# Performance work log

Hardware: AMD Instinct MI355X
Metric: run time of the kernel (lower is better)

The kernel has to match this reference:

```python
import jax, jax.numpy as jnp
import numpy as np

N_NODES = 50000
N_EDGES = 800000
N_GRAPHS = 64
IN_C, HID, OUT_C = 128, 96, 96
EPS = 1e-5


def gcn_conv(x, W, b, src, dst, n_nodes):
    # PyG GCNConv: linear -> symmetric-normalized aggregation with self-loops
    h = x @ W  # [N, C]
    deg = jax.ops.segment_sum(jnp.ones(src.shape[0], h.dtype), dst, num_segments=n_nodes) + 1.0  # +1 self-loop
    dinv = jax.lax.rsqrt(deg)  # deg >= 1, no inf
    norm = dinv[src] * dinv[dst]  # [E]
    agg = jax.ops.segment_sum(h[src] * norm[:, None], dst, num_segments=n_nodes)
    agg = agg + h * (dinv * dinv)[:, None]  # self-loop contribution
    return agg + b


def graph_norm(x, w, b, alpha, batch, n_graphs):
    # PyG GraphNorm: per-graph mean (scaled by learnable alpha) and variance
    cnt = jax.ops.segment_sum(jnp.ones(x.shape[0], x.dtype), batch, num_segments=n_graphs)[:, None]
    mean = jax.ops.segment_sum(x, batch, num_segments=n_graphs) / cnt
    xc = x - alpha * mean[batch]
    var = jax.ops.segment_sum(xc * xc, batch, num_segments=n_graphs) / cnt
    return w * xc * jax.lax.rsqrt(var[batch] + EPS) + b


def setup_inputs() -> dict:
    key = jax.random.key(0)
    ks = jax.random.split(key, 8)
    x = jax.random.normal(ks[0], (N_NODES, IN_C), jnp.float32)
    edge_index = jax.random.randint(ks[1], (2, N_EDGES), 0, N_NODES, jnp.int64)
    batch = jnp.sort(jax.random.randint(ks[2], (N_NODES,), 0, N_GRAPHS, jnp.int64))
    s1 = 1.0 / np.sqrt(IN_C)
    s2 = 1.0 / np.sqrt(HID)
    return {
        "x": x,
        "edge_index": edge_index,
        "batch": batch,
        "W1": jax.random.uniform(ks[3], (IN_C, HID), jnp.float32, -s1, s1),
        "b1": jnp.zeros((HID,), jnp.float32),
        "gn1_w": jnp.ones((HID,), jnp.float32),
        "gn1_b": jnp.zeros((HID,), jnp.float32),
        "gn1_a": jnp.ones((HID,), jnp.float32),
        "W2": jax.random.uniform(ks[4], (HID, OUT_C), jnp.float32, -s2, s2),
        "b2": jnp.zeros((OUT_C,), jnp.float32),
        "gn2_w": jnp.ones((OUT_C,), jnp.float32),
        "gn2_b": jnp.zeros((OUT_C,), jnp.float32),
        "gn2_a": jnp.ones((OUT_C,), jnp.float32),
    }


def reference(x, edge_index, batch, W1, b1, gn1_w, gn1_b, gn1_a, W2, b2, gn2_w, gn2_b, gn2_a):
    src, dst = edge_index[0], edge_index[1]
    h = gcn_conv(x, W1, b1, src, dst, N_NODES)
    h = graph_norm(h, gn1_w, gn1_b, gn1_a, batch, N_GRAPHS)
    h = jax.nn.relu(h)  # dropout = identity in eval mode
    h = gcn_conv(h, W2, b2, src, dst, N_NODES)
    h = graph_norm(h, gn2_w, gn2_b, gn2_a, batch, N_GRAPHS)
    h = jax.nn.relu(h)
    return h
```

## Files before the change

### kernel.cpp

```cpp
#include <hip/hip_runtime.h>
#include <hip/hip_bf16.h>

#define N_NODES 50000
#define N_EDGES 800000
#define N_GRAPHS 64
#define IN_C 128
#define HID 96
#define SLICES 8
#define NBUCK 196
#define NCHK 200
#define EPC 4000

typedef short s16x8 __attribute__((ext_vector_type(8)));
typedef float f32x4 __attribute__((ext_vector_type(4)));

__device__ inline unsigned short f2bf(float f) {
    union { __hip_bfloat16 b; unsigned short u; } cv;
    cv.b = __float2bfloat16(f);
    return cv.u;
}
__device__ inline float bf2f(unsigned short u) { return __uint_as_float((unsigned int)u << 16); }
__device__ inline float bf_lo(unsigned int u) { return __uint_as_float(u << 16); }
__device__ inline float bf_hi(unsigned int u) { return __uint_as_float(u & 0xffff0000u); }


__global__ void bounds_kernel(const int* __restrict__ batch, int* __restrict__ gstart,
                              int* __restrict__ gend, int n) {
    int i = blockIdx.x * blockDim.x + threadIdx.x;
    if (i >= n) return;
    int g = batch[i];
    if (i == 0) {
        gstart[g] = 0;
    } else {
        int gp = batch[i - 1];
        if (gp != g) { gstart[g] = i; gend[gp] = i - 1; }
    }
    if (i == n - 1) gend[g] = n - 1;
}

__global__ __launch_bounds__(256)
void p1_hist(const int* __restrict__ dst, int* __restrict__ chunkHist) {
    __shared__ int h[NBUCK];
    int c = blockIdx.x, t = threadIdx.x;
    for (int i = t; i < NBUCK; i += 256) h[i] = 0;
    __syncthreads();
    int base = c * EPC;
    for (int i = t; i < EPC; i += 256)
        atomicAdd(&h[dst[base + i] >> 8], 1);
    __syncthreads();
    for (int i = t; i < NBUCK; i += 256) chunkHist[c * NBUCK + i] = h[i];
}

__global__ __launch_bounds__(256)
void p2_offsets(const int* __restrict__ chunkHist, int* __restrict__ offTab,
                int* __restrict__ bucketBase, int* __restrict__ rowstart) {
    __shared__ int sh[256];
    int t = threadIdx.x;
    int tot = 0;
    if (t < NBUCK)
        for (int c = 0; c < NCHK; ++c) tot += chunkHist[c * NBUCK + t];
    sh[t] = (t < NBUCK) ? tot : 0;
    __syncthreads();
    for (int off = 1; off < 256; off <<= 1) {
        int x = (t >= off) ? sh[t - off] : 0;
        __syncthreads();
        sh[t] += x;
        __syncthreads();
    }
    if (t < NBUCK) {
        int bb = sh[t] - tot;
        bucketBase[t] = bb;
        int run = bb;
        for (int c = 0; c < NCHK; ++c) {
            offTab[c * NBUCK + t] = run;
            run += chunkHist[c * NBUCK + t];
        }
    }
    if (t == 0) { bucketBase[NBUCK] = N_EDGES; rowstart[N_NODES] = N_EDGES; }
}

__global__ __launch_bounds__(256)
void p3_place(const int* __restrict__ src, const int* __restrict__ dst,
              const int* __restrict__ offTab, unsigned int* __restrict__ epacked) {
    __shared__ int cur[NBUCK];
    int c = blockIdx.x, t = threadIdx.x;
    for (int i = t; i < NBUCK; i += 256) cur[i] = offTab[c * NBUCK + i];
    __syncthreads();
    int base = c * EPC;
    for (int i = t; i < EPC; i += 256) {
        int d = dst[base + i];
        int s = src[base + i];
        int pos = atomicAdd(&cur[d >> 8], 1);
        epacked[pos] = ((unsigned)(d & 255) << 16) | (unsigned)s;
    }
}

__global__ __launch_bounds__(256)
void p4_fine(const unsigned int* __restrict__ epacked, const int* __restrict__ bucketBase,
             int* __restrict__ rowstart, float* __restrict__ dinv,
             unsigned short* __restrict__ e_src16) {
    __shared__ int h[256];
    __shared__ int rs[256];
    __shared__ unsigned short sorted[8192];
    int b = blockIdx.x, t = threadIdx.x;
    int s0 = bucketBase[b], len = bucketBase[b + 1] - s0;
    h[t] = 0;
    __syncthreads();
    for (int i = t; i < len; i += 256)
        atomicAdd(&h[(epacked[s0 + i] >> 16) & 255], 1);
    __syncthreads();
    int deg = h[t];
    int v = deg;
    rs[t] = v;
    __syncthreads();
    for (int off = 1; off < 256; off <<= 1) {
        int x = (t >= off) ? rs[t - off] : 0;
        __syncthreads();
        rs[t] += x;
        __syncthreads();
    }
    int myrow = rs[t] - deg;
    int node = b * 256 + t;
    if (node < N_NODES) {
        rowstart[node] = s0 + myrow;
        dinv[node] = rsqrtf((float)deg + 1.0f);
    }
    __syncthreads();
    h[t] = myrow;
    __syncthreads();
    for (int i = t; i < len; i += 256) {
        unsigned int p = epacked[s0 + i];
        int pos = atomicAdd(&h[(p >> 16) & 255], 1);
        sorted[pos] = (unsigned short)(p & 0xffffu);
    }
    __syncthreads();
    for (int i = t; i < len; i += 256) e_src16[s0 + i] = sorted[i];
}

template <int K, bool PRENORM>
__global__ __launch_bounds__(256)
void gemm_mfma(const void* __restrict__ Xv, const float* __restrict__ W,
               const float* __restrict__ dinv, const int* __restrict__ batch,
               const float* __restrict__ gA, const float* __restrict__ gB,
               unsigned short* __restrict__ Hp) {
    constexpr int KP = K + 8;
    constexpr int KS = K / 32;
    __shared__ unsigned short Wt[96 * KP];
    int tid = threadIdx.x;
    for (int idx = tid; idx < K * 96; idx += 256) {
        int k = idx / 96, c = idx - k * 96;
        Wt[c * KP + k] = f2bf(W[idx]);
    }
    __syncthreads();

    const int lane = tid & 63;
    const int quad = lane >> 4;
    const int l16 = lane & 15;

    s16x8 Bf[6][KS];
#pragma unroll
    for (int t = 0; t < 6; ++t)
#pragma unroll
        for (int s = 0; s < KS; ++s)
            Bf[t][s] = *(const s16x8*)&Wt[(t * 16 + l16) * KP + s * 32 + quad * 8];

    int gw = blockIdx.x * 4 + (tid >> 6);
    int nw = gridDim.x * 4;
    for (int tile = gw; tile < N_NODES / 16; tile += nw) {
        int n0 = tile * 16;
        int row = n0 + l16;
        s16x8 Af[KS];
        if (!PRENORM) {
            const float* Xr = (const float*)Xv + (size_t)row * K;
#pragma unroll
            for (int s = 0; s < KS; ++s) {
                int k0 = s * 32 + quad * 8;
                float4 u = *(const float4*)(Xr + k0);
                float4 v = *(const float4*)(Xr + k0 + 4);
                s16x8 a;
                a[0] = (short)f2bf(u.x); a[1] = (short)f2bf(u.y);
                a[2] = (short)f2bf(u.z); a[3] = (short)f2bf(u.w);
                a[4] = (short)f2bf(v.x); a[5] = (short)f2bf(v.y);
                a[6] = (short)f2bf(v.z); a[7] = (short)f2bf(v.w);
                Af[s] = a;
            }
        } else {
            const unsigned short* Xr = (const unsigned short*)Xv + (size_t)row * HID;
            int g = batch[row];
            const float* ga = gA + g * HID;
            const float* gb = gB + g * HID;
#pragma unroll
            for (int s = 0; s < KS; ++s) {
                int k0 = s * 32 + quad * 8;
                uint4 raw = *(const uint4*)(Xr + k0);
                float4 a0 = *(const float4*)(ga + k0);
                float4 a1 = *(const float4*)(ga + k0 + 4);
                float4 b0 = *(const float4*)(gb + k0);
                float4 b1 = *(const float4*)(gb + k0 + 4);
                s16x8 a;
                a[0] = (short)f2bf(fmaxf(fmaf(bf_lo(raw.x), a0.x, b0.x), 0.f));
                a[1] = (short)f2bf(fmaxf(fmaf(bf_hi(raw.x), a0.y, b0.y), 0.f));
                a[2] = (short)f2bf(fmaxf(fmaf(bf_lo(raw.y), a0.z, b0.z), 0.f));
                a[3] = (short)f2bf(fmaxf(fmaf(bf_hi(raw.y), a0.w, b0.w), 0.f));
                a[4] = (short)f2bf(fmaxf(fmaf(bf_lo(raw.z), a1.x, b1.x), 0.f));
                a[5] = (short)f2bf(fmaxf(fmaf(bf_hi(raw.z), a1.y, b1.y), 0.f));
                a[6] = (short)f2bf(fmaxf(fmaf(bf_lo(raw.w), a1.z, b1.z), 0.f));
                a[7] = (short)f2bf(fmaxf(fmaf(bf_hi(raw.w), a1.w, b1.w), 0.f));
                Af[s] = a;
            }
        }
        f32x4 acc[6];
#pragma unroll
        for (int t = 0; t < 6; ++t) { acc[t][0] = 0.f; acc[t][1] = 0.f; acc[t][2] = 0.f; acc[t][3] = 0.f; }
#pragma unroll
        for (int s = 0; s < KS; ++s)
#pragma unroll
            for (int t = 0; t < 6; ++t)
                acc[t] = __builtin_amdgcn_mfma_f32_16x16x32_bf16(Af[s], Bf[t][s], acc[t], 0, 0, 0);

        float4 dv = *(const float4*)(dinv + n0 + quad * 4);
#pragma unroll
        for (int t = 0; t < 6; ++t) {
            size_t base = (size_t)(n0 + quad * 4) * HID + t * 16 + l16;
            Hp[base]            = f2bf(acc[t][0] * dv.x);
            Hp[base + HID]      = f2bf(acc[t][1] * dv.y);
            Hp[base + 2 * HID]  = f2bf(acc[t][2] * dv.z);
            Hp[base + 3 * HID]  = f2bf(acc[t][3] * dv.w);
        }
    }
}

__global__ __launch_bounds__(384)
void agg_kernel(const int* __restrict__ rowstart, const unsigned short* __restrict__ e_src,
                const float* __restrict__ dinv, const unsigned short* __restrict__ H,
                const float* __restrict__ bias, unsigned short* __restrict__ OUT) {
    int node = blockIdx.x * 16 + threadIdx.y;
    int x = threadIdx.x;
    const ushort4* H4 = (const ushort4*)H;
    size_t ridx = (size_t)node * 24 + x;
    ushort4 hv = H4[ridx];
    float ax = bf2f(hv.x), ay = bf2f(hv.y), az = bf2f(hv.z), aw = bf2f(hv.w);
    int s0 = rowstart[node], s1 = rowstart[node + 1];
    int i = s0;
    for (; i + 2 <= s1; i += 2) {
        int sA = e_src[i], sB = e_src[i + 1];
        ushort4 a4 = H4[(size_t)sA * 24 + x];
        ushort4 b4 = H4[(size_t)sB * 24 + x];
        ax += bf2f(a4.x); ay += bf2f(a4.y); az += bf2f(a4.z); aw += bf2f(a4.w);
        ax += bf2f(b4.x); ay += bf2f(b4.y); az += bf2f(b4.z); aw += bf2f(b4.w);
    }
    if (i < s1) {
        int sA = e_src[i];
        ushort4 a4 = H4[(size_t)sA * 24 + x];
        ax += bf2f(a4.x); ay += bf2f(a4.y); az += bf2f(a4.z); aw += bf2f(a4.w);
    }
    float di = dinv[node];
    float4 bb = ((const float4*)bias)[x];
    ushort4 ov;
    ov.x = f2bf(fmaf(ax, di, bb.x));
    ov.y = f2bf(fmaf(ay, di, bb.y));
    ov.z = f2bf(fmaf(az, di, bb.z));
    ov.w = f2bf(fmaf(aw, di, bb.w));
    ((ushort4*)OUT)[ridx] = ov;
}


__global__ __launch_bounds__(768)
void gn_partial(const unsigned short* __restrict__ Xb, const int* __restrict__ gstart,
                const int* __restrict__ gend, float* __restrict__ gSum, float* __restrict__ gSq) {
    __shared__ float4 sSum[32][24];
    __shared__ float4 sSq[32][24];
    int g = blockIdx.x, sl = blockIdx.y;
    int x = threadIdx.x, ty = threadIdx.y;
    int s = gstart[g], e = gend[g];
    float sx = 0, sy = 0, sz = 0, sw = 0, qx = 0, qy = 0, qz = 0, qw = 0;
    if (s <= e) {
        int cnt = e - s + 1;
        int per = (cnt + SLICES - 1) / SLICES;
        int n0 = s + sl * per;
        int n1 = min(n0 + per - 1, e);
        const ushort4* X4 = (const ushort4*)Xb;
        for (int n = n0 + ty; n <= n1; n += 32) {
            ushort4 h = X4[(size_t)n * 24 + x];
            float vx = bf2f(h.x), vy = bf2f(h.y), vz = bf2f(h.z), vw = bf2f(h.w);
            sx += vx; qx = fmaf(vx, vx, qx);
            sy += vy; qy = fmaf(vy, vy, qy);
            sz += vz; qz = fmaf(vz, vz, qz);
            sw += vw; qw = fmaf(vw, vw, qw);
        }
    }
    sSum[ty][x] = make_float4(sx, sy, sz, sw);
    sSq[ty][x] = make_float4(qx, qy, qz, qw);
    __syncthreads();
    for (int off = 16; off > 0; off >>= 1) {
        if (ty < off) {
            float4 a = sSum[ty + off][x], b = sSum[ty][x];
            sSum[ty][x] = make_float4(a.x + b.x, a.y + b.y, a.z + b.z, a.w + b.w);
            float4 c = sSq[ty + off][x], d = sSq[ty][x];
            sSq[ty][x] = make_float4(c.x + d.x, c.y + d.y, c.z + d.z, c.w + d.w);
        }
        __syncthreads();
    }
    if (ty == 0 && s <= e) {
        float4 S = sSum[0][x], Q = sSq[0][x];
        atomicAdd(&gSum[g * HID + x * 4 + 0], S.x);
        atomicAdd(&gSum[g * HID + x * 4 + 1], S.y);
        atomicAdd(&gSum[g * HID + x * 4 + 2], S.z);
        atomicAdd(&gSum[g * HID + x * 4 + 3], S.w);
        atomicAdd(&gSq[g * HID + x * 4 + 0], Q.x);
        atomicAdd(&gSq[g * HID + x * 4 + 1], Q.y);
        atomicAdd(&gSq[g * HID + x * 4 + 2], Q.z);
        atomicAdd(&gSq[g * HID + x * 4 + 3], Q.w);
    }
}

__global__ void gn_finalize(const float* __restrict__ gSum, const float* __restrict__ gSq,
                            const int* __restrict__ gstart, const int* __restrict__ gend,
                            const float* __restrict__ w, const float* __restrict__ b,
                            const float* __restrict__ a, float* __restrict__ gA,
                            float* __restrict__ gB) {
    int g = blockIdx.x, c = threadIdx.x;
    int s = gstart[g], e = gend[g];
    float A = 0.f, B = 0.f;
    if (s <= e) {
        float cnt = (float)(e - s + 1);
        float mean = gSum[g * HID + c] / cnt;
        float alpha = a[c];
        float var = gSq[g * HID + c] / cnt - (2.f * alpha - alpha * alpha) * mean * mean;
        var = fmaxf(var, 0.f);
        float rs = rsqrtf(var + 1e-5f);
        A = w[c] * rs;
        B = b[c] - alpha * mean * A;
    }
    gA[g * HID + c] = A;
    gB[g * HID + c] = B;
}

__global__ void gn_apply(const unsigned short* __restrict__ Xb, const int* __restrict__ batch,
                         const float* __restrict__ gA, const float* __restrict__ gB,
                         float* __restrict__ Y) {
    int n = blockIdx.x * 16 + threadIdx.y;
    int x = threadIdx.x;
    int g = batch[n];
    ushort4 h = ((const ushort4*)Xb)[(size_t)n * 24 + x];
    float4 a4 = ((const float4*)(gA + g * HID))[x];
    float4 b4 = ((const float4*)(gB + g * HID))[x];
    float4 v;
    v.x = fmaxf(fmaf(bf2f(h.x), a4.x, b4.x), 0.f);
    v.y = fmaxf(fmaf(bf2f(h.y), a4.y, b4.y), 0.f);
    v.z = fmaxf(fmaf(bf2f(h.z), a4.z, b4.z), 0.f);
    v.w = fmaxf(fmaf(bf2f(h.w), a4.w, b4.w), 0.f);
    ((float4*)Y)[(size_t)n * 24 + x] = v;
}

extern "C" void kernel_launch(void* const* d_in, const int* in_sizes, int n_in,
                              void* d_out, int out_size, void* d_ws, size_t ws_size,
                              hipStream_t stream) {
    const float* x     = (const float*)d_in[0];
    const int*   edge  = (const int*)d_in[1];
    const int*   batch = (const int*)d_in[2];
    const float* W1    = (const float*)d_in[3];
    const float* b1    = (const float*)d_in[4];
    const float* gn1_w = (const float*)d_in[5];
    const float* gn1_b = (const float*)d_in[6];
    const float* gn1_a = (const float*)d_in[7];
    const float* W2    = (const float*)d_in[8];
    const float* b2    = (const float*)d_in[9];
    const float* gn2_w = (const float*)d_in[10];
    const float* gn2_b = (const float*)d_in[11];
    const float* gn2_a = (const float*)d_in[12];
    float* out = (float*)d_out;

    const int* srcv = edge;
    const int* dstv = edge + N_EDGES;

    float* ws   = (float*)d_ws;
    float* dinv = ws;
    float* gSum = dinv + 50048;
    float* gSq  = gSum + 6144;
    float* gA   = gSq + 6144;
    float* gB   = gA + 6144;
    int* rowstart   = (int*)(gB + 6144);
    int* chunkHist  = rowstart + 50008;
    int* offTab     = chunkHist + NCHK * NBUCK;
    int* bucketBase = offTab + NCHK * NBUCK;
    int* gstart     = bucketBase + 200;
    int* gend       = gstart + 64;
    unsigned int* epacked = (unsigned int*)(gend + 64);
    unsigned short* e_src16 = (unsigned short*)(epacked + N_EDGES);
    unsigned short* Hbf = e_src16 + N_EDGES;
    unsigned short* Obf = Hbf + (size_t)N_NODES * HID;

    hipMemsetAsync(gstart, 0x7F, N_GRAPHS * sizeof(int), stream);
    hipMemsetAsync(gend, 0, N_GRAPHS * sizeof(int), stream);

    bounds_kernel<<<(N_NODES + 255) / 256, 256, 0, stream>>>(batch, gstart, gend, N_NODES);
    p1_hist<<<NCHK, 256, 0, stream>>>(dstv, chunkHist);
    p2_offsets<<<1, 256, 0, stream>>>(chunkHist, offTab, bucketBase, rowstart);
    p3_place<<<NCHK, 256, 0, stream>>>(srcv, dstv, offTab, epacked);
    p4_fine<<<NBUCK, 256, 0, stream>>>(epacked, bucketBase, rowstart, dinv, e_src16);

    const dim3 blk24x16(24, 16);
    const dim3 blk24x32(24, 32);
    const int nodeGrid16 = N_NODES / 16;

    gemm_mfma<IN_C, false><<<256, 256, 0, stream>>>(x, W1, dinv, nullptr, nullptr, nullptr, Hbf);
    agg_kernel<<<nodeGrid16, blk24x16, 0, stream>>>(rowstart, e_src16, dinv, Hbf, b1, Obf);
    hipMemsetAsync(gSum, 0, 2 * 6144 * sizeof(float), stream);
    gn_partial<<<dim3(N_GRAPHS, SLICES), blk24x32, 0, stream>>>(Obf, gstart, gend, gSum, gSq);
    gn_finalize<<<N_GRAPHS, HID, 0, stream>>>(gSum, gSq, gstart, gend, gn1_w, gn1_b, gn1_a, gA, gB);

    gemm_mfma<HID, true><<<256, 256, 0, stream>>>(Obf, W2, dinv, batch, gA, gB, Hbf);
    agg_kernel<<<nodeGrid16, blk24x16, 0, stream>>>(rowstart, e_src16, dinv, Hbf, b2, Obf);
    hipMemsetAsync(gSum, 0, 2 * 6144 * sizeof(float), stream);
    gn_partial<<<dim3(N_GRAPHS, SLICES), blk24x32, 0, stream>>>(Obf, gstart, gend, gSum, gSq);
    gn_finalize<<<N_GRAPHS, HID, 0, stream>>>(gSum, gSq, gstart, gend, gn2_w, gn2_b, gn2_a, gA, gB);
    gn_apply<<<nodeGrid16, blk24x16, 0, stream>>>(Obf, batch, gA, gB, out);
}
```

Baseline: 170.0 us.

## Fuse graph bounds, GraphNorm finalize, parallelize offset scan, widen aggregation vectors

Folds the graph-bounds computation into the histogram kernel and splits the single-block offset computation into a per-bucket parallel scan plus a small base scan. The GraphNorm finalize step moves into gn_partial through a last-block-done atomic counter, and the separate memsets collapse into one. Aggregation and apply kernels now load 8 bf16 values per thread with 4-way unrolled gathers, and the GEMM grid size changes. This cuts launch count and the serial 200-iteration loop, at the cost of extra atomics and fence ordering.

```diff
diff --git a/kernel.cpp b/kernel.cpp
--- a/kernel.cpp
+++ b/kernel.cpp
@@ -22,24 +22,20 @@
 __device__ inline float bf2f(unsigned short u) { return __uint_as_float((unsigned int)u << 16); }
 __device__ inline float bf_lo(unsigned int u) { return __uint_as_float(u << 16); }
 __device__ inline float bf_hi(unsigned int u) { return __uint_as_float(u & 0xffff0000u); }
-
-
-__global__ void bounds_kernel(const int* __restrict__ batch, int* __restrict__ gstart,
-                              int* __restrict__ gend, int n) {
-    int i = blockIdx.x * blockDim.x + threadIdx.x;
-    if (i >= n) return;
-    int g = batch[i];
-    if (i == 0) {
-        gstart[g] = 0;
-    } else {
-        int gp = batch[i - 1];
-        if (gp != g) { gstart[g] = i; gend[gp] = i - 1; }
-    }
-    if (i == n - 1) gend[g] = n - 1;
-}
-
-__global__ __launch_bounds__(256)
-void p1_hist(const int* __restrict__ dst, int* __restrict__ chunkHist) {
+__device__ inline unsigned int pack2(float lo, float hi) {
+    return (unsigned)f2bf(lo) | ((unsigned)f2bf(hi) << 16);
+}
+__device__ inline void acc8(float* a, uint4 r) {
+    a[0] += bf_lo(r.x); a[1] += bf_hi(r.x);
+    a[2] += bf_lo(r.y); a[3] += bf_hi(r.y);
+    a[4] += bf_lo(r.z); a[5] += bf_hi(r.z);
+    a[6] += bf_lo(r.w); a[7] += bf_hi(r.w);
+}
+
+
+__global__ __launch_bounds__(256)
+void p1_hist(const int* __restrict__ dst, int* __restrict__ chunkHist,
+             const int* __restrict__ batch, int* __restrict__ gstart, int* __restrict__ gend) {
     __shared__ int h[NBUCK];
     int c = blockIdx.x, t = threadIdx.x;
     for (int i = t; i < NBUCK; i += 256) h[i] = 0;
@@ -49,17 +45,47 @@
         atomicAdd(&h[dst[base + i] >> 8], 1);
     __syncthreads();
     for (int i = t; i < NBUCK; i += 256) chunkHist[c * NBUCK + i] = h[i];
-}
-
-__global__ __launch_bounds__(256)
-void p2_offsets(const int* __restrict__ chunkHist, int* __restrict__ offTab,
-                int* __restrict__ bucketBase, int* __restrict__ rowstart) {
+
+    int gi = c * 256 + t;
+    if (gi < N_NODES) {
+        int g = batch[gi];
+        if (gi == 0) {
+            gstart[g] = 0;
+        } else {
+            int gp = batch[gi - 1];
+            if (gp != g) { gstart[g] = gi; gend[gp] = gi - 1; }
+        }
+        if (gi == N_NODES - 1) gend[g] = N_NODES - 1;
+    }
+}
+
+__global__ __launch_bounds__(256)
+void p2a_scan(const int* __restrict__ chunkHist, int* __restrict__ offTabRel,
+              int* __restrict__ bucketTot) {
+    __shared__ int sh[256];
+    __shared__ int hv[256];
+    int b = blockIdx.x, t = threadIdx.x;
+    int v = (t < NCHK) ? chunkHist[t * NBUCK + b] : 0;
+    hv[t] = v;
+    sh[t] = v;
+    __syncthreads();
+    for (int off = 1; off < 256; off <<= 1) {
+        int x = (t >= off) ? sh[t - off] : 0;
+        __syncthreads();
+        sh[t] += x;
+        __syncthreads();
+    }
+    if (t < NCHK) offTabRel[t * NBUCK + b] = sh[t] - hv[t];
+    if (t == 255) bucketTot[b] = sh[255];
+}
+
+__global__ __launch_bounds__(256)
+void p2b_base(const int* __restrict__ bucketTot, int* __restrict__ bucketBase,
+              int* __restrict__ rowstart) {
     __shared__ int sh[256];
     int t = threadIdx.x;
-    int tot = 0;
-    if (t < NBUCK)
-        for (int c = 0; c < NCHK; ++c) tot += chunkHist[c * NBUCK + t];
-    sh[t] = (t < NBUCK) ? tot : 0;
+    int v = (t < NBUCK) ? bucketTot[t] : 0;
+    sh[t] = v;
     __syncthreads();
     for (int off = 1; off < 256; off <<= 1) {
         int x = (t >= off) ? sh[t - off] : 0;
@@ -67,24 +93,18 @@
         sh[t] += x;
         __syncthreads();
     }
-    if (t < NBUCK) {
-        int bb = sh[t] - tot;
-        bucketBase[t] = bb;
-        int run = bb;
-        for (int c = 0; c < NCHK; ++c) {
-            offTab[c * NBUCK + t] = run;
-            run += chunkHist[c * NBUCK + t];
-        }
-    }
+    if (t < NBUCK) bucketBase[t] = sh[t] - v;
     if (t == 0) { bucketBase[NBUCK] = N_EDGES; rowstart[N_NODES] = N_EDGES; }
 }
 
 __global__ __launch_bounds__(256)
 void p3_place(const int* __restrict__ src, const int* __restrict__ dst,
-              const int* __restrict__ offTab, unsigned int* __restrict__ epacked) {
+              const int* __restrict__ offTabRel, const int* __restrict__ bucketBase,
+              unsigned int* __restrict__ epacked) {
     __shared__ int cur[NBUCK];
     int c = blockIdx.x, t = threadIdx.x;
-    for (int i = t; i < NBUCK; i += 256) cur[i] = offTab[c * NBUCK + i];
+    for (int i = t; i < NBUCK; i += 256)
+        cur[i] = bucketBase[i] + offTabRel[c * NBUCK + i];
     __syncthreads();
     int base = c * EPC;
     for (int i = t; i < EPC; i += 256) {
@@ -110,8 +130,7 @@
         atomicAdd(&h[(epacked[s0 + i] >> 16) & 255], 1);
     __syncthreads();
     int deg = h[t];
-    int v = deg;
-    rs[t] = v;
+    rs[t] = deg;
     __syncthreads();
     for (int off = 1; off < 256; off <<= 1) {
         int x = (t >= off) ? rs[t - off] : 0;
@@ -234,42 +253,45 @@
 void agg_kernel(const int* __restrict__ rowstart, const unsigned short* __restrict__ e_src,
                 const float* __restrict__ dinv, const unsigned short* __restrict__ H,
                 const float* __restrict__ bias, unsigned short* __restrict__ OUT) {
-    int node = blockIdx.x * 16 + threadIdx.y;
+    int node = blockIdx.x * 32 + threadIdx.y;
+    if (node >= N_NODES) return;
     int x = threadIdx.x;
-    const ushort4* H4 = (const ushort4*)H;
-    size_t ridx = (size_t)node * 24 + x;
-    ushort4 hv = H4[ridx];
-    float ax = bf2f(hv.x), ay = bf2f(hv.y), az = bf2f(hv.z), aw = bf2f(hv.w);
+    const uint4* H8 = (const uint4*)H;
+    size_t ridx = (size_t)node * 12 + x;
+    float a[8] = {0, 0, 0, 0, 0, 0, 0, 0};
+    acc8(a, H8[ridx]);
     int s0 = rowstart[node], s1 = rowstart[node + 1];
     int i = s0;
-    for (; i + 2 <= s1; i += 2) {
-        int sA = e_src[i], sB = e_src[i + 1];
-        ushort4 a4 = H4[(size_t)sA * 24 + x];
-        ushort4 b4 = H4[(size_t)sB * 24 + x];
-        ax += bf2f(a4.x); ay += bf2f(a4.y); az += bf2f(a4.z); aw += bf2f(a4.w);
-        ax += bf2f(b4.x); ay += bf2f(b4.y); az += bf2f(b4.z); aw += bf2f(b4.w);
-    }
-    if (i < s1) {
-        int sA = e_src[i];
-        ushort4 a4 = H4[(size_t)sA * 24 + x];
-        ax += bf2f(a4.x); ay += bf2f(a4.y); az += bf2f(a4.z); aw += bf2f(a4.w);
-    }
+    for (; i + 4 <= s1; i += 4) {
+        int sA = e_src[i], sB = e_src[i + 1], sC = e_src[i + 2], sD = e_src[i + 3];
+        uint4 rA = H8[(size_t)sA * 12 + x];
+        uint4 rB = H8[(size_t)sB * 12 + x];
+        uint4 rC = H8[(size_t)sC * 12 + x];
+        uint4 rD = H8[(size_t)sD * 12 + x];
+        acc8(a, rA); acc8(a, rB); acc8(a, rC); acc8(a, rD);
+    }
+    for (; i < s1; ++i)
+        acc8(a, H8[(size_t)e_src[i] * 12 + x]);
+
     float di = dinv[node];
-    float4 bb = ((const float4*)bias)[x];
-    ushort4 ov;
-    ov.x = f2bf(fmaf(ax, di, bb.x));
-    ov.y = f2bf(fmaf(ay, di, bb.y));
-    ov.z = f2bf(fmaf(az, di, bb.z));
-    ov.w = f2bf(fmaf(aw, di, bb.w));
-    ((ushort4*)OUT)[ridx] = ov;
-}
-
+    float4 b0 = *(const float4*)(bias + x * 8);
+    float4 b1 = *(const float4*)(bias + x * 8 + 4);
+    uint4 ov;
+    ov.x = pack2(fmaf(a[0], di, b0.x), fmaf(a[1], di, b0.y));
+    ov.y = pack2(fmaf(a[2], di, b0.z), fmaf(a[3], di, b0.w));
+    ov.z = pack2(fmaf(a[4], di, b1.x), fmaf(a[5], di, b1.y));
+    ov.w = pack2(fmaf(a[6], di, b1.z), fmaf(a[7], di, b1.w));
+    ((uint4*)OUT)[ridx] = ov;
+}
 
 __global__ __launch_bounds__(768)
 void gn_partial(const unsigned short* __restrict__ Xb, const int* __restrict__ gstart,
-                const int* __restrict__ gend, float* __restrict__ gSum, float* __restrict__ gSq) {
+                const int* __restrict__ gend, float* __restrict__ gSum, float* __restrict__ gSq,
+                int* __restrict__ done, const float* __restrict__ w, const float* __restrict__ b,
+                const float* __restrict__ a, float* __restrict__ gA, float* __restrict__ gB) {
     __shared__ float4 sSum[32][24];
     __shared__ float4 sSq[32][24];
+    __shared__ int lastFlag;
     int g = blockIdx.x, sl = blockIdx.y;
     int x = threadIdx.x, ty = threadIdx.y;
     int s = gstart[g], e = gend[g];
@@ -294,14 +316,14 @@
     __syncthreads();
     for (int off = 16; off > 0; off >>= 1) {
         if (ty < off) {
-            float4 a = sSum[ty + off][x], b = sSum[ty][x];
-            sSum[ty][x] = make_float4(a.x + b.x, a.y + b.y, a.z + b.z, a.w + b.w);
-            float4 c = sSq[ty + off][x], d = sSq[ty][x];
-            sSq[ty][x] = make_float4(c.x + d.x, c.y + d.y, c.z + d.z, c.w + d.w);
-        }
-        __syncthreads();
-    }
-    if (ty == 0 && s <= e) {
+            float4 A = sSum[ty + off][x], B = sSum[ty][x];
+            sSum[ty][x] = make_float4(A.x + B.x, A.y + B.y, A.z + B.z, A.w + B.w);
+            float4 C = sSq[ty + off][x], D = sSq[ty][x];
+            sSq[ty][x] = make_float4(C.x + D.x, C.y + D.y, C.z + D.z, C.w + D.w);
+        }
+        __syncthreads();
+    }
+    if (ty == 0) {
         float4 S = sSum[0][x], Q = sSq[0][x];
         atomicAdd(&gSum[g * HID + x * 4 + 0], S.x);
         atomicAdd(&gSum[g * HID + x * 4 + 1], S.y);
@@ -311,46 +333,61 @@
         atomicAdd(&gSq[g * HID + x * 4 + 1], Q.y);
         atomicAdd(&gSq[g * HID + x * 4 + 2], Q.z);
         atomicAdd(&gSq[g * HID + x * 4 + 3], Q.w);
-    }
-}
-
-__global__ void gn_finalize(const float* __restrict__ gSum, const float* __restrict__ gSq,
-                            const int* __restrict__ gstart, const int* __restrict__ gend,
-                            const float* __restrict__ w, const float* __restrict__ b,
-                            const float* __restrict__ a, float* __restrict__ gA,
-                            float* __restrict__ gB) {
-    int g = blockIdx.x, c = threadIdx.x;
-    int s = gstart[g], e = gend[g];
-    float A = 0.f, B = 0.f;
-    if (s <= e) {
-        float cnt = (float)(e - s + 1);
-        float mean = gSum[g * HID + c] / cnt;
-        float alpha = a[c];
-        float var = gSq[g * HID + c] / cnt - (2.f * alpha - alpha * alpha) * mean * mean;
-        var = fmaxf(var, 0.f);
-        float rs = rsqrtf(var + 1e-5f);
-        A = w[c] * rs;
-        B = b[c] - alpha * mean * A;
-    }
-    gA[g * HID + c] = A;
-    gB[g * HID + c] = B;
-}
-
-__global__ void gn_apply(const unsigned short* __restrict__ Xb, const int* __restrict__ batch,
-                         const float* __restrict__ gA, const float* __restrict__ gB,
-                         float* __restrict__ Y) {
-    int n = blockIdx.x * 16 + threadIdx.y;
+        __threadfence();
+    }
+    __syncthreads();
+    if (ty == 0 && x == 0) {
+        int old = atomicAdd(&done[g], 1);
+        lastFlag = (old == SLICES - 1) ? 1 : 0;
+    }
+    __syncthreads();
+    if (lastFlag) {
+        int t = ty * 24 + x;
+        if (t < HID) {
+            float S = atomicAdd(&gSum[g * HID + t], 0.0f);
+            float Q = atomicAdd(&gSq[g * HID + t], 0.0f);
+            float A = 0.f, B = 0.f;
+            if (s <= e) {
+                float cnt = (float)(e - s + 1);
+                float mean = S / cnt;
+                float alpha = a[t];
+                float var = Q / cnt - (2.f * alpha - alpha * alpha) * mean * mean;
+                var = fmaxf(var, 0.f);
+                float rsv = rsqrtf(var + 1e-5f);
+                A = w[t] * rsv;
+                B = b[t] - alpha * mean * A;
+            }
+            gA[g * HID + t] = A;
+            gB[g * HID + t] = B;
+        }
+    }
+}
+
+__global__ __launch_bounds__(384)
+void gn_apply(const unsigned short* __restrict__ Xb, const int* __restrict__ batch,
+              const float* __restrict__ gA, const float* __restrict__ gB,
+              float* __restrict__ Y) {
+    int n = blockIdx.x * 32 + threadIdx.y;
+    if (n >= N_NODES) return;
     int x = threadIdx.x;
     int g = batch[n];
-    ushort4 h = ((const ushort4*)Xb)[(size_t)n * 24 + x];
-    float4 a4 = ((const float4*)(gA + g * HID))[x];
-    float4 b4 = ((const float4*)(gB + g * HID))[x];
-    float4 v;
-    v.x = fmaxf(fmaf(bf2f(h.x), a4.x, b4.x), 0.f);
-    v.y = fmaxf(fmaf(bf2f(h.y), a4.y, b4.y), 0.f);
-    v.z = fmaxf(fmaf(bf2f(h.z), a4.z, b4.z), 0.f);
-    v.w = fmaxf(fmaf(bf2f(h.w), a4.w, b4.w), 0.f);
-    ((float4*)Y)[(size_t)n * 24 + x] = v;
+    uint4 h = ((const uint4*)Xb)[(size_t)n * 12 + x];
+    const float* ga = gA + g * HID + x * 8;
+    const float* gb = gB + g * HID + x * 8;
+    float4 a0 = *(const float4*)ga, a1 = *(const float4*)(ga + 4);
+    float4 b0 = *(const float4*)gb, b1 = *(const float4*)(gb + 4);
+    float4 o0, o1;
+    o0.x = fmaxf(fmaf(bf_lo(h.x), a0.x, b0.x), 0.f);
+    o0.y = fmaxf(fmaf(bf_hi(h.x), a0.y, b0.y), 0.f);
+    o0.z = fmaxf(fmaf(bf_lo(h.y), a0.z, b0.z), 0.f);
+    o0.w = fmaxf(fmaf(bf_hi(h.y), a0.w, b0.w), 0.f);
+    o1.x = fmaxf(fmaf(bf_lo(h.z), a1.x, b1.x), 0.f);
+    o1.y = fmaxf(fmaf(bf_hi(h.z), a1.y, b1.y), 0.f);
+    o1.z = fmaxf(fmaf(bf_lo(h.w), a1.z, b1.z), 0.f);
+    o1.w = fmaxf(fmaf(bf_hi(h.w), a1.w, b1.w), 0.f);
+    float* yr = Y + (size_t)n * HID + x * 8;
+    *(float4*)yr = o0;
+    *(float4*)(yr + 4) = o1;
 }
 
 extern "C" void kernel_launch(void* const* d_in, const int* in_sizes, int n_in,
@@ -376,44 +413,47 @@
 
     float* ws   = (float*)d_ws;
     float* dinv = ws;
-    float* gSum = dinv + 50048;
-    float* gSq  = gSum + 6144;
-    float* gA   = gSq + 6144;
+    float* gA   = dinv + 50048;
     float* gB   = gA + 6144;
-    int* rowstart   = (int*)(gB + 6144);
+    float* zb    = gB + 6144;
+    float* gSum1 = zb;
+    float* gSq1  = gSum1 + 6144;
+    float* gSum2 = gSq1 + 6144;
+    float* gSq2  = gSum2 + 6144;
+    int* done1   = (int*)(gSq2 + 6144);
+    int* done2   = done1 + 64;
+    int* gstart  = done2 + 64;
+    int* gend    = gstart + 64;
+    const size_t ZB_BYTES = (4 * 6144 + 4 * 64) * sizeof(float);
+    int* rowstart   = gend + 64;
     int* chunkHist  = rowstart + 50008;
-    int* offTab     = chunkHist + NCHK * NBUCK;
-    int* bucketBase = offTab + NCHK * NBUCK;
-    int* gstart     = bucketBase + 200;
-    int* gend       = gstart + 64;
-    unsigned int* epacked = (unsigned int*)(gend + 64);
+    int* offTabRel  = chunkHist + NCHK * NBUCK;
+    int* bucketTot  = offTabRel + NCHK * NBUCK;
+    int* bucketBase = bucketTot + 200;
+    unsigned int* epacked = (unsigned int*)(bucketBase + 200);
     unsigned short* e_src16 = (unsigned short*)(epacked + N_EDGES);
     unsigned short* Hbf = e_src16 + N_EDGES;
     unsigned short* Obf = Hbf + (size_t)N_NODES * HID;
 
-    hipMemsetAsync(gstart, 0x7F, N_GRAPHS * sizeof(int), stream);
-    hipMemsetAsync(gend, 0, N_GRAPHS * sizeof(int), stream);
-
-    bounds_kernel<<<(N_NODES + 255) / 256, 256, 0, stream>>>(batch, gstart, gend, N_NODES);
-    p1_hist<<<NCHK, 256, 0, stream>>>(dstv, chunkHist);
-    p2_offsets<<<1, 256, 0, stream>>>(chunkHist, offTab, bucketBase, rowstart);
-    p3_place<<<NCHK, 256, 0, stream>>>(srcv, dstv, offTab, epacked);
+    hipMemsetAsync(zb, 0, ZB_BYTES, stream);
+    p1_hist<<<NCHK, 256, 0, stream>>>(dstv, chunkHist, batch, gstart, gend);
+    p2a_scan<<<NBUCK, 256, 0, stream>>>(chunkHist, offTabRel, bucketTot);
+    p2b_base<<<1, 256, 0, stream>>>(bucketTot, bucketBase, rowstart);
+    p3_place<<<NCHK, 256, 0, stream>>>(srcv, dstv, offTabRel, bucketBase, epacked);
     p4_fine<<<NBUCK, 256, 0, stream>>>(epacked, bucketBase, rowstart, dinv, e_src16);
 
-    const dim3 blk24x16(24, 16);
+    const dim3 blk12x32(12, 32);
     const dim3 blk24x32(24, 32);
-    const int nodeGrid16 = N_NODES / 16;
-
-    gemm_mfma<IN_C, false><<<256, 256, 0, stream>>>(x, W1, dinv, nullptr, nullptr, nullptr, Hbf);
-    agg_kernel<<<nodeGrid16, blk24x16, 0, stream>>>(rowstart, e_src16, dinv, Hbf, b1, Obf);
-    hipMemsetAsync(gSum, 0, 2 * 6144 * sizeof(float), stream);
-    gn_partial<<<dim3(N_GRAPHS, SLICES), blk24x32, 0, stream>>>(Obf, gstart, gend, gSum, gSq);
-    gn_finalize<<<N_GRAPHS, HID, 0, stream>>>(gSum, gSq, gstart, gend, gn1_w, gn1_b, gn1_a, gA, gB);
-
-    gemm_mfma<HID, true><<<256, 256, 0, stream>>>(Obf, W2, dinv, batch, gA, gB, Hbf);
-    agg_kernel<<<nodeGrid16, blk24x16, 0, stream>>>(rowstart, e_src16, dinv, Hbf, b2, Obf);
-    hipMemsetAsync(gSum, 0, 2 * 6144 * sizeof(float), stream);
-    gn_partial<<<dim3(N_GRAPHS, SLICES), blk24x32, 0, stream>>>(Obf, gstart, gend, gSum, gSq);
-    gn_finalize<<<N_GRAPHS, HID, 0, stream>>>(gSum, gSq, gstart, gend, gn2_w, gn2_b, gn2_a, gA, gB);
-    gn_apply<<<nodeGrid16, blk24x16, 0, stream>>>(Obf, batch, gA, gB, out);
-}
+    const int nodeGrid32 = (N_NODES + 31) / 32;
+
+    gemm_mfma<IN_C, false><<<391, 256, 0, stream>>>(x, W1, dinv, nullptr, nullptr, nullptr, Hbf);
+    agg_kernel<<<nodeGrid32, blk12x32, 0, stream>>>(rowstart, e_src16, dinv, Hbf, b1, Obf);
+    gn_partial<<<dim3(N_GRAPHS, SLICES), blk24x32, 0, stream>>>(Obf, gstart, gend, gSum1, gSq1,
+                                                                done1, gn1_w, gn1_b, gn1_a, gA, gB);
+
+    gemm_mfma<HID, true><<<391, 256, 0, stream>>>(Obf, W2, dinv, batch, gA, gB, Hbf);
+    agg_kernel<<<nodeGrid32, blk12x32, 0, stream>>>(rowstart, e_src16, dinv, Hbf, b2, Obf);
+    gn_partial<<<dim3(N_GRAPHS, SLICES), blk24x32, 0, stream>>>(Obf, gstart, gend, gSum2, gSq2,
+                                                                done2, gn2_w, gn2_b, gn2_a, gA, gB);
+    gn_apply<<<nodeGrid32, blk12x32, 0, stream>>>(Obf, batch, gA, gB, out);
+}
```

Measured after the change: 153.7 us. 9.6% less time.
